# Kernel tuning notes

Measured on AMD Instinct MI355X. Metric: run time of the kernel, lower is better.

The kernel has to match this reference:

```python
import jax, jax.numpy as jnp
import numpy as np

D_MODEL = 1024
HIDDEN = 4096
N_EXPERTS = 8
LB_COEF = 0.01
B, N = 2, 2048


def setup_inputs() -> dict:
    key = jax.random.key(0)
    k_x, k_g, k_w1, k_w2 = jax.random.split(key, 4)
    s = 0.02
    return {
        "x": jax.random.normal(k_x, (B, N, D_MODEL), dtype=jnp.float32),
        "gate_w": jax.random.normal(k_g, (N_EXPERTS, D_MODEL), dtype=jnp.float32) * s,
        "w1": jax.random.normal(k_w1, (N_EXPERTS, HIDDEN, D_MODEL), dtype=jnp.float32) * s,  # torch Linear weight [out,in]
        "b1": jnp.zeros((N_EXPERTS, HIDDEN), dtype=jnp.float32),
        "w2": jax.random.normal(k_w2, (N_EXPERTS, D_MODEL, HIDDEN), dtype=jnp.float32) * s,
        "b2": jnp.zeros((N_EXPERTS, D_MODEL), dtype=jnp.float32),
    }


def reference(x, gate_w, w1, b1, w2, b2):
    # gate logits: Linear(d_model, E, bias=False)
    logits = jnp.einsum('bnd,ed->bne', x, gate_w)
    probs = jax.nn.softmax(logits, axis=-1)            # router_prob
    gate_scores = jnp.max(probs, axis=-1)              # top-1 prob [B,N]
    sel = jnp.argmax(probs, axis=-1)                   # selected expert [B,N]

    # load-balance aux loss
    onehot = jax.nn.one_hot(sel, N_EXPERTS, dtype=x.dtype)
    f = onehot.mean(axis=(0, 1))                       # fraction of tokens per expert
    P = probs.mean(axis=(0, 1))                        # mean router prob per expert
    aux_loss = LB_COEF * N_EXPERTS * jnp.sum(f * P)

    # dispatch: loop over fixed small expert count (structurally distinct weights)
    out = jnp.zeros_like(x)
    for e in range(N_EXPERTS):
        h = jax.nn.gelu(jnp.einsum('bnd,hd->bnh', x, w1[e]) + b1[e], approximate=False)
        y = jnp.einsum('bnh,dh->bnd', h, w2[e]) + b2[e]
        out = out + jnp.where((sel == e)[..., None], gate_scores[..., None] * y, jnp.zeros((), x.dtype))
    return out, aux_loss
```

## Files before the change

### kernel.cpp

```cpp
#include <hip/hip_runtime.h>
#include <math.h>

#define T_TOK 4096
#define DM 1024
#define HID 4096
#define NEXP 8

typedef unsigned short u16;
typedef __attribute__((ext_vector_type(8))) short short8;
typedef __attribute__((ext_vector_type(4))) float f32x4;

__device__ __forceinline__ u16 f2bf(float f){
  unsigned u = __float_as_uint(f);
  u += 0x7FFF + ((u >> 16) & 1);
  return (u16)(u >> 16);
}
__device__ __forceinline__ float bf2f(u16 b){
  return __uint_as_float(((unsigned)b) << 16);
}

#define GATE_OFF   0u
#define CNT_OFF    16384u
#define LIST_OFF   16512u
#define PROBS_OFF  147584u
#define XB_OFF     278656u
#define H_OFF      8667264u

__global__ void zero_cnt_kernel(int* cnt){
  if (threadIdx.x < NEXP) cnt[threadIdx.x] = 0;
}

__global__ __launch_bounds__(256) void gate_kernel(
    const float* __restrict__ x, const float* __restrict__ gw,
    float* __restrict__ gateo, int* __restrict__ cnt, int* __restrict__ list,
    float* __restrict__ probs, u16* __restrict__ xb)
{
  int tid = threadIdx.x;
  int lane = tid & 63;
  int w = tid >> 6;
  int t = blockIdx.x * 4 + w;

  const float4* x4 = (const float4*)(x + (size_t)t * DM);
  const float4* g4 = (const float4*)gw;

  float acc[8] = {0,0,0,0,0,0,0,0};
  #pragma unroll
  for (int i = 0; i < 4; i++){
    int p = i * 64 + lane;
    float4 xv = x4[p];
    ushort4 pk;
    pk.x = f2bf(xv.x); pk.y = f2bf(xv.y); pk.z = f2bf(xv.z); pk.w = f2bf(xv.w);
    *(ushort4*)&xb[(size_t)t * DM + (size_t)p * 4] = pk;
    #pragma unroll
    for (int e = 0; e < NEXP; e++){
      float4 gv = g4[e * 256 + p];
      acc[e] += xv.x * gv.x + xv.y * gv.y + xv.z * gv.z + xv.w * gv.w;
    }
  }
  #pragma unroll
  for (int e = 0; e < NEXP; e++){
    #pragma unroll
    for (int off = 32; off; off >>= 1)
      acc[e] += __shfl_xor(acc[e], off);
  }
  if (lane == 0){
    float mx = acc[0];
    #pragma unroll
    for (int e = 1; e < NEXP; e++) mx = fmaxf(mx, acc[e]);
    float p[8]; float s = 0.f;
    #pragma unroll
    for (int e = 0; e < NEXP; e++){ p[e] = expf(acc[e] - mx); s += p[e]; }
    float inv = 1.f / s;
    int be = 0; float bp = p[0];
    #pragma unroll
    for (int e = 1; e < NEXP; e++){ if (p[e] > bp){ bp = p[e]; be = e; } }
    #pragma unroll
    for (int e = 0; e < NEXP; e++) probs[(size_t)t * 8 + e] = p[e] * inv;
    gateo[t] = bp * inv;
    int pos = atomicAdd(&cnt[be], 1);
    list[be * T_TOK + pos] = t;
  }
}

__global__ __launch_bounds__(256) void aux_kernel(
    const float* __restrict__ probs, const int* __restrict__ cnt,
    float* __restrict__ aux_out)
{
  __shared__ float sm[256 * 8];
  int tid = threadIdx.x;
  float s[8] = {0,0,0,0,0,0,0,0};
  for (int i = 0; i < 16; i++){
    int t = i * 256 + tid;
    #pragma unroll
    for (int e = 0; e < 8; e++) s[e] += probs[(size_t)t * 8 + e];
  }
  #pragma unroll
  for (int e = 0; e < 8; e++) sm[tid * 8 + e] = s[e];
  __syncthreads();
  for (int st = 128; st; st >>= 1){
    if (tid < st){
      #pragma unroll
      for (int e = 0; e < 8; e++) sm[tid * 8 + e] += sm[(tid + st) * 8 + e];
    }
    __syncthreads();
  }
  if (tid == 0){
    float a = 0.f;
    #pragma unroll
    for (int e = 0; e < 8; e++){
      float f = (float)cnt[e] / (float)T_TOK;
      float P = sm[e] / (float)T_TOK;
      a += f * P;
    }
    aux_out[0] = 0.01f * (float)NEXP * a;
  }
}

template<int KT, int NTOT, bool PHASE2>
__global__ __launch_bounds__(256, 2) void ffn_gemm(
    const u16*  __restrict__ Aall,
    const float* __restrict__ Ball,
    const float* __restrict__ bias,
    const int*  __restrict__ cnt,
    const int*  __restrict__ list,
    const float* __restrict__ gate,
    u16*  __restrict__ hOut,
    float* __restrict__ yOut)
{
  constexpr int NT = NTOT / 128;
  int bid = blockIdx.x;
  int e  = bid / (32 * NT);
  int r  = bid % (32 * NT);
  int mt = r / NT, nt = r % NT;
  int ne = cnt[e];
  int m0 = mt * 128;
  if (m0 >= ne) return;
  const int*   lst = list + e * T_TOK;
  const float* B   = Ball + (size_t)e * NTOT * KT;
  const float* bi  = bias + (size_t)e * NTOT;
  int n0 = nt * 128;

  __shared__ u16 As[128 * 64];
  __shared__ u16 Bs[128 * 64];

  int tid  = threadIdx.x;
  int lane = tid & 63;
  int w    = tid >> 6;
  int wr = (w >> 1) * 64, wc = (w & 1) * 64;
  int fr = lane & 15, fq = lane >> 4;

  const u16*  aSrc[4]; int dstA[4];
  const float* bSrc[4]; int dstB[4];
  #pragma unroll
  for (int i = 0; i < 4; i++){
    int idx = i * 256 + tid;
    int row = idx >> 3, ch = idx & 7;
    int g = ch ^ (row & 7);
    int mrow = m0 + row; if (mrow > ne - 1) mrow = ne - 1;
    int tok = lst[mrow];
    aSrc[i] = Aall + (size_t)tok * KT + g * 8;
    dstA[i] = row * 64 + ch * 8;
    bSrc[i] = B + (size_t)(n0 + row) * KT + g * 8;
    dstB[i] = row * 64 + ch * 8;
  }

  f32x4 acc[4][4];
  #pragma unroll
  for (int m = 0; m < 4; m++)
    #pragma unroll
    for (int n = 0; n < 4; n++)
      acc[m][n] = (f32x4){0.f, 0.f, 0.f, 0.f};

  for (int ks = 0; ks < KT / 64; ++ks){
    if (ks) __syncthreads();
    int ko = ks * 64;
    #pragma unroll
    for (int i = 0; i < 4; i++){
      *(uint4*)&As[dstA[i]] = *(const uint4*)(aSrc[i] + ko);
    }
    #pragma unroll
    for (int i = 0; i < 4; i++){
      const float4* s = (const float4*)(bSrc[i] + ko);
      float4 f0 = s[0], f1 = s[1];
      uint4 p;
      p.x = (unsigned)f2bf(f0.x) | ((unsigned)f2bf(f0.y) << 16);
      p.y = (unsigned)f2bf(f0.z) | ((unsigned)f2bf(f0.w) << 16);
      p.z = (unsigned)f2bf(f1.x) | ((unsigned)f2bf(f1.y) << 16);
      p.w = (unsigned)f2bf(f1.z) | ((unsigned)f2bf(f1.w) << 16);
      *(uint4*)&Bs[dstB[i]] = p;
    }
    __syncthreads();
    #pragma unroll
    for (int kc = 0; kc < 2; kc++){
      short8 a[4], b[4];
      #pragma unroll
      for (int m = 0; m < 4; m++){
        int row = wr + m * 16 + fr;
        int slot = (kc * 4 + fq) ^ (row & 7);
        a[m] = *(const short8*)&As[row * 64 + slot * 8];
      }
      #pragma unroll
      for (int n = 0; n < 4; n++){
        int row = wc + n * 16 + fr;
        int slot = (kc * 4 + fq) ^ (row & 7);
        b[n] = *(const short8*)&Bs[row * 64 + slot * 8];
      }
      #pragma unroll
      for (int m = 0; m < 4; m++)
        #pragma unroll
        for (int n = 0; n < 4; n++)
          acc[m][n] = __builtin_amdgcn_mfma_f32_16x16x32_bf16(a[m], b[n], acc[m][n], 0, 0, 0);
    }
  }

  #pragma unroll
  for (int n = 0; n < 4; n++){
    int col = n0 + wc + n * 16 + fr;
    float bv = bi[col];
    #pragma unroll
    for (int m = 0; m < 4; m++){
      int rbase = m0 + wr + m * 16 + fq * 4;
      f32x4 v = acc[m][n];
      #pragma unroll
      for (int i = 0; i < 4; i++){
        int mrow = rbase + i;
        if (mrow < ne){
          int tok = lst[mrow];
          float val = v[i] + bv;
          if (PHASE2){
            yOut[(size_t)tok * NTOT + col] = gate[tok] * val;
          } else {
            float gl = 0.5f * val * (1.0f + erff(val * 0.70710678118654752f));
            hOut[(size_t)tok * NTOT + col] = f2bf(gl);
          }
        }
      }
    }
  }
}

extern "C" void kernel_launch(void* const* d_in, const int* in_sizes, int n_in,
                              void* d_out, int out_size, void* d_ws, size_t ws_size,
                              hipStream_t stream) {
  const float* x   = (const float*)d_in[0];
  const float* gw  = (const float*)d_in[1];
  const float* w1  = (const float*)d_in[2];
  const float* b1  = (const float*)d_in[3];
  const float* w2  = (const float*)d_in[4];
  const float* b2  = (const float*)d_in[5];

  char* ws = (char*)d_ws;
  float* gateo = (float*)(ws + GATE_OFF);
  int*   cnt   = (int*)  (ws + CNT_OFF);
  int*   list  = (int*)  (ws + LIST_OFF);
  float* probs = (float*)(ws + PROBS_OFF);
  u16*   xb    = (u16*)  (ws + XB_OFF);
  u16*   h     = (u16*)  (ws + H_OFF);

  float* out = (float*)d_out;
  float* aux = out + (size_t)T_TOK * DM;

  hipLaunchKernelGGL(zero_cnt_kernel, dim3(1), dim3(64), 0, stream, cnt);
  hipLaunchKernelGGL(gate_kernel, dim3(T_TOK / 4), dim3(256), 0, stream,
                     x, gw, gateo, cnt, list, probs, xb);
  hipLaunchKernelGGL(aux_kernel, dim3(1), dim3(256), 0, stream, probs, cnt, aux);
  hipLaunchKernelGGL((ffn_gemm<DM, HID, false>), dim3(NEXP * 32 * (HID / 128)), dim3(256), 0, stream,
                     xb, w1, b1, cnt, list, gateo, h, (float*)nullptr);
  hipLaunchKernelGGL((ffn_gemm<HID, DM, true>), dim3(NEXP * 32 * (DM / 128)), dim3(256), 0, stream,
                     h, w2, b2, cnt, list, gateo, (u16*)nullptr, out);
}
```

Before: 354.7 us.

## Pre-convert weights to bf16, enlarge GEMM tiles, double-buffer via direct-to-LDS loads, split-K phase 2

Expert weights are converted to bf16 once per call in separate kernels, so the GEMM inner loop no longer converts fp32 B tiles. The FFN GEMM now uses 256x256 tiles with 512 threads and double-buffered LDS filled by global_load_lds. The second GEMM uses a 4-way split-K writing fp32 partials, followed by a reduce kernel that sums them and applies the gate. This adds extra full passes over the weights for conversion and more workspace traffic for the partials. The large tiles cut parallelism when experts receive few tokens.

```diff
diff --git a/kernel.cpp b/kernel.cpp
--- a/kernel.cpp
+++ b/kernel.cpp
@@ -14,9 +14,6 @@
   unsigned u = __float_as_uint(f);
   u += 0x7FFF + ((u >> 16) & 1);
   return (u16)(u >> 16);
-}
-__device__ __forceinline__ float bf2f(u16 b){
-  return __uint_as_float(((unsigned)b) << 16);
 }
 
 #define GATE_OFF   0u
@@ -25,9 +22,31 @@
 #define PROBS_OFF  147584u
 #define XB_OFF     278656u
 #define H_OFF      8667264u
+#define W1B_OFF    42221696u
+#define PART_OFF   W1B_OFF
+#define W2B_OFF    109330560u
+#define WS_NEED_BF 176439424u
+
+__device__ __forceinline__ void glds16(const void* g, void* l){
+  __builtin_amdgcn_global_load_lds((const __attribute__((address_space(1))) void*)g,
+                                   (__attribute__((address_space(3))) void*)l, 16, 0, 0);
+}
 
 __global__ void zero_cnt_kernel(int* cnt){
   if (threadIdx.x < NEXP) cnt[threadIdx.x] = 0;
+}
+
+__global__ __launch_bounds__(256) void cvt_kernel(const float* __restrict__ src,
+                                                  u16* __restrict__ dst){
+  size_t i = (size_t)blockIdx.x * 256 + threadIdx.x;
+  const float4* s = (const float4*)src + i * 2;
+  float4 a = s[0], b = s[1];
+  uint4 p;
+  p.x = (unsigned)f2bf(a.x) | ((unsigned)f2bf(a.y) << 16);
+  p.y = (unsigned)f2bf(a.z) | ((unsigned)f2bf(a.w) << 16);
+  p.z = (unsigned)f2bf(b.x) | ((unsigned)f2bf(b.y) << 16);
+  p.w = (unsigned)f2bf(b.z) | ((unsigned)f2bf(b.w) << 16);
+  ((uint4*)dst)[i] = p;
 }
 
 __global__ __launch_bounds__(256) void gate_kernel(
@@ -116,110 +135,110 @@
   }
 }
 
-template<int KT, int NTOT, bool PHASE2>
-__global__ __launch_bounds__(256, 2) void ffn_gemm(
+template<int NTOT, int ASTR, int BSTR, int NSPLIT, bool PHASE2>
+__global__ __launch_bounds__(512, 2) void ffn_gemm(
     const u16*  __restrict__ Aall,
-    const float* __restrict__ Ball,
+    const u16*  __restrict__ Bb,
     const float* __restrict__ bias,
     const int*  __restrict__ cnt,
     const int*  __restrict__ list,
-    const float* __restrict__ gate,
     u16*  __restrict__ hOut,
-    float* __restrict__ yOut)
+    float* __restrict__ pOut)
 {
-  constexpr int NT = NTOT / 128;
+  constexpr int NT = NTOT / 256;
+  constexpr int KS = 16;
   int bid = blockIdx.x;
-  int e  = bid / (32 * NT);
-  int r  = bid % (32 * NT);
-  int mt = r / NT, nt = r % NT;
+  int nt = bid % NT;
+  int t1 = bid / NT;
+  int sk = t1 % NSPLIT;
+  int t2 = t1 / NSPLIT;
+  int mt = t2 % 16;
+  int e  = t2 / 16;
   int ne = cnt[e];
-  int m0 = mt * 128;
+  int m0 = mt * 256;
   if (m0 >= ne) return;
-  const int*   lst = list + e * T_TOK;
-  const float* B   = Ball + (size_t)e * NTOT * KT;
-  const float* bi  = bias + (size_t)e * NTOT;
-  int n0 = nt * 128;
-
-  __shared__ u16 As[128 * 64];
-  __shared__ u16 Bs[128 * 64];
+  const int* lst = list + e * T_TOK;
+  int n0 = nt * 256;
+  int koff = sk * 1024;
+
+  __shared__ u16 As[2][16384];
+  __shared__ u16 Bs[2][16384];
 
   int tid  = threadIdx.x;
   int lane = tid & 63;
   int w    = tid >> 6;
-  int wr = (w >> 1) * 64, wc = (w & 1) * 64;
+  int wm = w >> 2, wn = w & 3;
   int fr = lane & 15, fq = lane >> 4;
 
-  const u16*  aSrc[4]; int dstA[4];
-  const float* bSrc[4]; int dstB[4];
+  const u16* aS[4]; const u16* bS[4];
   #pragma unroll
   for (int i = 0; i < 4; i++){
-    int idx = i * 256 + tid;
-    int row = idx >> 3, ch = idx & 7;
-    int g = ch ^ (row & 7);
-    int mrow = m0 + row; if (mrow > ne - 1) mrow = ne - 1;
-    int tok = lst[mrow];
-    aSrc[i] = Aall + (size_t)tok * KT + g * 8;
-    dstA[i] = row * 64 + ch * 8;
-    bSrc[i] = B + (size_t)(n0 + row) * KT + g * 8;
-    dstB[i] = row * 64 + ch * 8;
-  }
-
-  f32x4 acc[4][4];
-  #pragma unroll
-  for (int m = 0; m < 4; m++)
+    int seg = w * 4 + i;
+    int r   = seg * 8 + (lane >> 3);
+    int g   = (lane & 7) ^ (r & 7);
+    int mrow = m0 + r; if (mrow > ne - 1) mrow = ne - 1;
+    aS[i] = Aall + (size_t)lst[mrow] * ASTR + koff + g * 8;
+    bS[i] = Bb + (size_t)e * NTOT * BSTR + (size_t)(n0 + r) * BSTR + koff + g * 8;
+  }
+
+  f32x4 acc[8][4];
+  #pragma unroll
+  for (int m = 0; m < 8; m++)
     #pragma unroll
     for (int n = 0; n < 4; n++)
       acc[m][n] = (f32x4){0.f, 0.f, 0.f, 0.f};
 
-  for (int ks = 0; ks < KT / 64; ++ks){
-    if (ks) __syncthreads();
-    int ko = ks * 64;
-    #pragma unroll
-    for (int i = 0; i < 4; i++){
-      *(uint4*)&As[dstA[i]] = *(const uint4*)(aSrc[i] + ko);
-    }
-    #pragma unroll
-    for (int i = 0; i < 4; i++){
-      const float4* s = (const float4*)(bSrc[i] + ko);
-      float4 f0 = s[0], f1 = s[1];
-      uint4 p;
-      p.x = (unsigned)f2bf(f0.x) | ((unsigned)f2bf(f0.y) << 16);
-      p.y = (unsigned)f2bf(f0.z) | ((unsigned)f2bf(f0.w) << 16);
-      p.z = (unsigned)f2bf(f1.x) | ((unsigned)f2bf(f1.y) << 16);
-      p.w = (unsigned)f2bf(f1.z) | ((unsigned)f2bf(f1.w) << 16);
-      *(uint4*)&Bs[dstB[i]] = p;
-    }
-    __syncthreads();
+  #pragma unroll
+  for (int i = 0; i < 4; i++){
+    int seg = w * 4 + i;
+    glds16(aS[i], &As[0][seg * 512]);
+    glds16(bS[i], &Bs[0][seg * 512]);
+  }
+  __syncthreads();
+
+  int buf = 0;
+  for (int ks = 0; ks < KS; ++ks){
+    if (ks + 1 < KS){
+      #pragma unroll
+      for (int i = 0; i < 4; i++){
+        int seg = w * 4 + i;
+        glds16(aS[i] + (ks + 1) * 64, &As[buf ^ 1][seg * 512]);
+        glds16(bS[i] + (ks + 1) * 64, &Bs[buf ^ 1][seg * 512]);
+      }
+    }
     #pragma unroll
     for (int kc = 0; kc < 2; kc++){
-      short8 a[4], b[4];
-      #pragma unroll
-      for (int m = 0; m < 4; m++){
-        int row = wr + m * 16 + fr;
+      short8 a[8], b[4];
+      #pragma unroll
+      for (int m = 0; m < 8; m++){
+        int row  = wm * 128 + m * 16 + fr;
         int slot = (kc * 4 + fq) ^ (row & 7);
-        a[m] = *(const short8*)&As[row * 64 + slot * 8];
+        a[m] = *(const short8*)&As[buf][row * 64 + slot * 8];
       }
       #pragma unroll
       for (int n = 0; n < 4; n++){
-        int row = wc + n * 16 + fr;
+        int row  = wn * 64 + n * 16 + fr;
         int slot = (kc * 4 + fq) ^ (row & 7);
-        b[n] = *(const short8*)&Bs[row * 64 + slot * 8];
+        b[n] = *(const short8*)&Bs[buf][row * 64 + slot * 8];
       }
       #pragma unroll
-      for (int m = 0; m < 4; m++)
+      for (int m = 0; m < 8; m++)
         #pragma unroll
         for (int n = 0; n < 4; n++)
           acc[m][n] = __builtin_amdgcn_mfma_f32_16x16x32_bf16(a[m], b[n], acc[m][n], 0, 0, 0);
     }
+    __syncthreads();
+    buf ^= 1;
   }
 
   #pragma unroll
   for (int n = 0; n < 4; n++){
-    int col = n0 + wc + n * 16 + fr;
-    float bv = bi[col];
-    #pragma unroll
-    for (int m = 0; m < 4; m++){
-      int rbase = m0 + wr + m * 16 + fq * 4;
+    int col = n0 + wn * 64 + n * 16 + fr;
+    float bv = bias[(size_t)e * NTOT + col];
+    if (PHASE2 && sk != 0) bv = 0.f;
+    #pragma unroll
+    for (int m = 0; m < 8; m++){
+      int rbase = m0 + wm * 128 + m * 16 + fq * 4;
       f32x4 v = acc[m][n];
       #pragma unroll
       for (int i = 0; i < 4; i++){
@@ -228,7 +247,7 @@
           int tok = lst[mrow];
           float val = v[i] + bv;
           if (PHASE2){
-            yOut[(size_t)tok * NTOT + col] = gate[tok] * val;
+            pOut[((size_t)sk * T_TOK + tok) * DM + col] = val;
           } else {
             float gl = 0.5f * val * (1.0f + erff(val * 0.70710678118654752f));
             hOut[(size_t)tok * NTOT + col] = f2bf(gl);
@@ -237,6 +256,23 @@
       }
     }
   }
+}
+
+__global__ __launch_bounds__(256) void reduce_kernel(
+    const float* __restrict__ part, const float* __restrict__ gate,
+    float* __restrict__ out)
+{
+  size_t i = (size_t)blockIdx.x * 256 + threadIdx.x;
+  constexpr size_t S = (size_t)T_TOK * DM / 4;
+  const float4* p = (const float4*)part;
+  float4 a = p[i], b = p[i + S], c = p[i + 2 * S], d = p[i + 3 * S];
+  float g = gate[i >> 8];
+  float4 o;
+  o.x = (a.x + b.x + c.x + d.x) * g;
+  o.y = (a.y + b.y + c.y + d.y) * g;
+  o.z = (a.z + b.z + c.z + d.z) * g;
+  o.w = (a.w + b.w + c.w + d.w) * g;
+  ((float4*)out)[i] = o;
 }
 
 extern "C" void kernel_launch(void* const* d_in, const int* in_sizes, int n_in,
@@ -256,16 +292,26 @@
   float* probs = (float*)(ws + PROBS_OFF);
   u16*   xb    = (u16*)  (ws + XB_OFF);
   u16*   h     = (u16*)  (ws + H_OFF);
+  u16*   w1b   = (u16*)  (ws + W1B_OFF);
+  float* part  = (float*)(ws + PART_OFF);
+  u16*   w2b   = (u16*)  (ws + W2B_OFF);
 
   float* out = (float*)d_out;
   float* aux = out + (size_t)T_TOK * DM;
 
   hipLaunchKernelGGL(zero_cnt_kernel, dim3(1), dim3(64), 0, stream, cnt);
+  hipLaunchKernelGGL(cvt_kernel, dim3(16384), dim3(256), 0, stream, w1, w1b);
+  hipLaunchKernelGGL(cvt_kernel, dim3(16384), dim3(256), 0, stream, w2, w2b);
   hipLaunchKernelGGL(gate_kernel, dim3(T_TOK / 4), dim3(256), 0, stream,
                      x, gw, gateo, cnt, list, probs, xb);
   hipLaunchKernelGGL(aux_kernel, dim3(1), dim3(256), 0, stream, probs, cnt, aux);
-  hipLaunchKernelGGL((ffn_gemm<DM, HID, false>), dim3(NEXP * 32 * (HID / 128)), dim3(256), 0, stream,
-                     xb, w1, b1, cnt, list, gateo, h, (float*)nullptr);
-  hipLaunchKernelGGL((ffn_gemm<HID, DM, true>), dim3(NEXP * 32 * (DM / 128)), dim3(256), 0, stream,
-                     h, w2, b2, cnt, list, gateo, (u16*)nullptr, out);
-}
+
+  hipLaunchKernelGGL((ffn_gemm<HID, DM, DM, 1, false>),
+                     dim3(NEXP * 16 * (HID / 256)), dim3(512), 0, stream,
+                     xb, w1b, b1, cnt, list, h, (float*)nullptr);
+  hipLaunchKernelGGL((ffn_gemm<DM, HID, HID, 4, true>),
+                     dim3(NEXP * 16 * (DM / 256) * 4), dim3(512), 0, stream,
+                     h, w2b, b2, cnt, list, (u16*)nullptr, part);
+  hipLaunchKernelGGL(reduce_kernel, dim3(T_TOK * DM / 4 / 256), dim3(256), 0, stream,
+                     part, gateo, out);
+}
```

Result: slower. 370.5 us (+4.4%).
